# Performance work log

Hardware: AMD Instinct MI355X
Metric: run time of the kernel (lower is better)

The kernel has to match this reference:

```python
import jax, jax.numpy as jnp
import numpy as np

B, S, D_IN = 2, 2048, 2048
N_HEADS, N_KV, HEAD_DIM = 16, 4, 128
GROUP = N_HEADS // N_KV  # 4
SCALING = 256.0 ** -0.5  # query_pre_attn_scalar = 256
EPS = 1e-6


def rms_norm(x, scale):
    # RMSNorm over last dim (head_dim)
    var = jnp.mean(jnp.square(x), axis=-1, keepdims=True)
    return x * jax.lax.rsqrt(var + EPS) * scale


def apply_rope(x, cos, sin):
    # x: [b, h, s, d]; cos/sin: [s, d]
    d = x.shape[-1]
    x1, x2 = x[..., : d // 2], x[..., d // 2 :]
    rotated = jnp.concatenate([-x2, x1], axis=-1)
    return x * cos[None, None, :, :] + rotated * sin[None, None, :, :]


def setup_inputs() -> dict:
    key = jax.random.key(0)
    ks = jax.random.split(key, 6)
    x = jax.random.normal(ks[0], (B, S, D_IN), dtype=jnp.float32)
    Wq = jax.random.normal(ks[1], (D_IN, N_HEADS * HEAD_DIM), dtype=jnp.float32) * 0.02
    Wk = jax.random.normal(ks[2], (D_IN, N_KV * HEAD_DIM), dtype=jnp.float32) * 0.02
    Wv = jax.random.normal(ks[3], (D_IN, N_KV * HEAD_DIM), dtype=jnp.float32) * 0.02
    Wo = jax.random.normal(ks[4], (N_HEADS * HEAD_DIM, D_IN), dtype=jnp.float32) * 0.02
    q_scale = jnp.ones((HEAD_DIM,), dtype=jnp.float32)
    k_scale = jnp.ones((HEAD_DIM,), dtype=jnp.float32)
    # RoPE tables: angles repeated twice across head_dim
    inv_freq = 1.0 / (10000.0 ** (np.arange(0, HEAD_DIM, 2, dtype=np.float32) / HEAD_DIM))
    angles = np.arange(S, dtype=np.float32)[:, None] * inv_freq[None, :]  # [S, d/2]
    angles = np.concatenate([angles, angles], axis=-1)  # [S, d]
    cos = jnp.asarray(np.cos(angles), dtype=jnp.float32)
    sin = jnp.asarray(np.sin(angles), dtype=jnp.float32)
    # causal mask: True = masked (future positions)
    mask = jnp.triu(jnp.ones((S, S), dtype=bool), k=1)
    return {"x": x, "mask": mask, "cos": cos, "sin": sin,
            "Wq": Wq, "Wk": Wk, "Wv": Wv, "Wo": Wo,
            "q_scale": q_scale, "k_scale": k_scale}


def reference(x, mask, cos, sin, Wq, Wk, Wv, Wo, q_scale, k_scale):
    b, s, _ = x.shape
    q = (x @ Wq).reshape(b, s, N_HEADS, HEAD_DIM).transpose(0, 2, 1, 3)  # [b,h,s,d]
    k = (x @ Wk).reshape(b, s, N_KV, HEAD_DIM).transpose(0, 2, 1, 3)     # [b,g,s,d]
    v = (x @ Wv).reshape(b, s, N_KV, HEAD_DIM).transpose(0, 2, 1, 3)
    # qk-norm
    q = rms_norm(q, q_scale)
    k = rms_norm(k, k_scale)
    # RoPE
    q = apply_rope(q, cos, sin)
    k = apply_rope(k, cos, sin)
    # repeat KV across groups
    k = jnp.repeat(k, GROUP, axis=1)  # [b,h,s,d]
    v = jnp.repeat(v, GROUP, axis=1)
    q = q * SCALING
    scores = jnp.einsum('bhqd,bhkd->bhqk', q, k)
    scores = jnp.where(mask, -jnp.inf, scores)
    weights = jax.nn.softmax(scores, axis=-1)
    ctx = jnp.einsum('bhqk,bhkd->bhqd', weights, v)
    ctx = ctx.transpose(0, 2, 1, 3).reshape(b, s, N_HEADS * HEAD_DIM)
    return ctx @ Wo
```

## Files before the change

### kernel.cpp

```cpp
#include <hip/hip_runtime.h>
#include <hip/hip_bf16.h>


using u16 = unsigned short;
using u32 = unsigned int;

constexpr int Ss  = 2048;
constexpr int Hh  = 16;
constexpr int KVH = 4;

typedef __attribute__((ext_vector_type(8))) short bf16x8;
typedef __attribute__((ext_vector_type(4))) float f32x4;

__device__ inline float b2f(u16 v)  { return __uint_as_float(((u32)v) << 16); }
__device__ inline u16 f2bf(float x) {
  u32 u = __float_as_uint(x);
  return (u16)((u + 0x7fffu + ((u >> 16) & 1u)) >> 16);
}

typedef const __attribute__((address_space(1))) unsigned int gas_u32;
typedef __attribute__((address_space(3))) unsigned int las_u32;
__device__ inline void gl16(const void* g, void* l) {
  __builtin_amdgcn_global_load_lds((gas_u32*)g, (las_u32*)l, 16, 0, 0);
}

__global__ __launch_bounds__(256) void cvt_bf16(const float* __restrict__ in,
                                                u16* __restrict__ out, int n4) {
  int i = blockIdx.x * 256 + threadIdx.x;
  if (i < n4) {
    float4 f = reinterpret_cast<const float4*>(in)[i];
    ushort4 o;
    o.x = f2bf(f.x); o.y = f2bf(f.y); o.z = f2bf(f.z); o.w = f2bf(f.w);
    reinterpret_cast<ushort4*>(out)[i] = o;
  }
}

__global__ __launch_bounds__(256) void tcvt(const float* __restrict__ in,
                                            u16* __restrict__ out, int N, int K) {
  __shared__ u16 T[64][66];
  const int k0 = blockIdx.x * 64, n0 = blockIdx.y * 64;
  const int c = threadIdx.x & 63, rb = threadIdx.x >> 6;
#pragma unroll
  for (int p = 0; p < 16; p++) {
    int r = p * 4 + rb;
    T[c][r] = f2bf(in[(size_t)(k0 + r) * N + n0 + c]);
  }
  __syncthreads();
#pragma unroll
  for (int p = 0; p < 16; p++) {
    int nr = p * 4 + rb;
    out[(size_t)(n0 + nr) * K + k0 + c] = T[nr][c];
  }
}

__global__ __launch_bounds__(256) void vtrans(const u16* __restrict__ kv,
                                              u16* __restrict__ vT) {
  __shared__ u16 T[64][66];
  const int s0 = blockIdx.x * 64, d0 = blockIdx.y * 64, z = blockIdx.z;
  const int b = z >> 2, kvh = z & 3;
  const int c = threadIdx.x & 63, rb = threadIdx.x >> 6;
#pragma unroll
  for (int p = 0; p < 16; p++) {
    int r = p * 4 + rb;
    T[c][r] = kv[(size_t)(b * Ss + s0 + r) * 1024 + 512 + kvh * 128 + d0 + c];
  }
  __syncthreads();
#pragma unroll
  for (int p = 0; p < 16; p++) {
    int dr = p * 4 + rb;
    vT[((size_t)z * 128 + d0 + dr) * Ss + s0 + c] = T[dr][c];
  }
}

template <int OUT_F32>
__global__ __launch_bounds__(256) void gemm_bt(const u16* __restrict__ A,
                                               const u16* __restrict__ Bt,
                                               void* __restrict__ C,
                                               int N, int K) {
  __shared__ u16 As[128 * 64];
  __shared__ u16 Bs[128 * 64];
  const int t = threadIdx.x, w = t >> 6, lane = t & 63;
  const int lrow = lane & 15, quad = lane >> 4;
  const int wm = w & 1, wn = w >> 1;
  const int m0 = blockIdx.x * 128, n0 = blockIdx.y * 128;

  f32x4 acc[4][4];
#pragma unroll
  for (int i = 0; i < 4; i++)
#pragma unroll
    for (int j = 0; j < 4; j++) acc[i][j] = (f32x4)0.f;

  const int srow = t >> 3;
  const int scol = (t & 7) * 8;

  for (int k0 = 0; k0 < K; k0 += 64) {
#pragma unroll
    for (int c = 0; c < 4; c++) {
      gl16(A + (size_t)(m0 + c * 32 + srow) * K + k0 + scol,
           (char*)As + c * 4096 + t * 16);
      gl16(Bt + (size_t)(n0 + c * 32 + srow) * K + k0 + scol,
           (char*)Bs + c * 4096 + t * 16);
    }
    __syncthreads();
#pragma unroll
    for (int kc = 0; kc < 2; kc++) {
      bf16x8 af[4], bfr[4];
#pragma unroll
      for (int i = 0; i < 4; i++) {
        af[i] = *reinterpret_cast<const bf16x8*>(
            &As[(wm * 64 + i * 16 + lrow) * 64 + kc * 32 + quad * 8]);
        bfr[i] = *reinterpret_cast<const bf16x8*>(
            &Bs[(wn * 64 + i * 16 + lrow) * 64 + kc * 32 + quad * 8]);
      }
#pragma unroll
      for (int mi = 0; mi < 4; mi++)
#pragma unroll
        for (int ni = 0; ni < 4; ni++)
          acc[mi][ni] =
              __builtin_amdgcn_mfma_f32_16x16x32_bf16(af[mi], bfr[ni], acc[mi][ni], 0, 0, 0);
    }
    __syncthreads();
  }

#pragma unroll
  for (int mi = 0; mi < 4; mi++)
#pragma unroll
    for (int ni = 0; ni < 4; ni++)
#pragma unroll
      for (int r = 0; r < 4; r++) {
        int row = m0 + wm * 64 + mi * 16 + quad * 4 + r;
        int col = n0 + wn * 64 + ni * 16 + lrow;
        if (OUT_F32)
          reinterpret_cast<float*>(C)[(size_t)row * N + col] = acc[mi][ni][r];
        else
          reinterpret_cast<u16*>(C)[(size_t)row * N + col] = f2bf(acc[mi][ni][r]);
      }
}

__global__ __launch_bounds__(256) void rmsrope2(u16* __restrict__ qbuf,
                                                u16* __restrict__ kvb,
                                                const float* __restrict__ qsc,
                                                const float* __restrict__ ksc,
                                                const float* __restrict__ cosb,
                                                const float* __restrict__ sinb) {
  const int w = threadIdx.x >> 6, lane = threadIdx.x & 63;
  const int vi = blockIdx.x * 4 + w;
  const int tok = vi / 20, j = vi - tok * 20;
  const int s = tok & (Ss - 1);
  const bool isq = j < 16;
  u16* p = isq ? (qbuf + (size_t)tok * 2048 + j * 128)
               : (kvb + (size_t)tok * 1024 + (j - 16) * 128);
  const float* scale = isq ? qsc : ksc;
  const float mult = isq ? 0.0625f : 1.0f;
  float e0 = b2f(p[lane]), e1 = b2f(p[lane + 64]);
  float ss = e0 * e0 + e1 * e1;
#pragma unroll
  for (int off = 32; off > 0; off >>= 1) ss += __shfl_xor(ss, off);
  float rr = rsqrtf(ss * (1.0f / 128.0f) + 1e-6f);
  float x0 = e0 * rr * scale[lane];
  float x1 = e1 * rr * scale[lane + 64];
  float c0 = cosb[s * 128 + lane], c1 = cosb[s * 128 + 64 + lane];
  float sn0 = sinb[s * 128 + lane], sn1 = sinb[s * 128 + 64 + lane];
  p[lane]      = f2bf((x0 * c0 - x1 * sn0) * mult);
  p[lane + 64] = f2bf((x1 * c1 + x0 * sn1) * mult);
}

__global__ __launch_bounds__(256, 2) void attn_mfma(const u16* __restrict__ qb,
                                                    const u16* __restrict__ kv,
                                                    const u16* __restrict__ vT,
                                                    u16* __restrict__ ctx) {
  __shared__ u16 Ks[2][64 * 128];
  __shared__ u16 Vs[2][128 * 64];
  __shared__ u16 Ps[4][32 * 40];
  const int i = blockIdx.x;
  const int qt = (i < 256) ? (15 - (i >> 5)) : ((i - 256) >> 5);
  const int hb = i & 31;
  const int h = hb & 15, b = hb >> 4;
  const int t = threadIdx.x, w = t >> 6, lane = t & 63;
  const int lrow = lane & 15, quad = lane >> 4;
  const int kvh = h >> 2;
  const int qw = qt * 128 + w * 32;

  const u16* kbase = kv + (size_t)b * Ss * 1024 + kvh * 128;
  const u16* vbase = vT + (size_t)(b * KVH + kvh) * 128 * Ss;

  const int kr  = t >> 4;
  const int kco = ((t & 15) ^ (kr & 7)) * 8;
  const int vr  = t >> 3;
  const int vco = ((t & 7) ^ (vr & 7)) * 8;
  const int sw8 = (lrow & 7) << 3;

  bf16x8 qf[2][4];
#pragma unroll
  for (int g = 0; g < 2; g++)
#pragma unroll
    for (int c = 0; c < 4; c++)
      qf[g][c] = *reinterpret_cast<const bf16x8*>(
          qb + ((size_t)(b * Ss + qw + g * 16 + lrow) * Hh + h) * 128 + c * 32 + quad * 8);

  f32x4 o[2][8];
#pragma unroll
  for (int g = 0; g < 2; g++)
#pragma unroll
    for (int n = 0; n < 8; n++) o[g][n] = (f32x4)0.f;
  float mx[2] = {-1e30f, -1e30f}, ls[2] = {0.f, 0.f};

  const int ntile = 2 * qt + 2;

#pragma unroll
  for (int p = 0; p < 4; p++) {
    gl16(kbase + (size_t)(p * 16 + kr) * 1024 + kco,
         (char*)Ks[0] + (p * 256 + t) * 16);
    gl16(vbase + (size_t)(p * 32 + vr) * Ss + vco,
         (char*)Vs[0] + (p * 256 + t) * 16);
  }
  __syncthreads();

  int cur = 0;
  for (int kt = 0; kt < ntile; kt++) {
    const int kb0 = kt * 64;
    if (kt + 1 < ntile) {
      const int nb0 = kb0 + 64;
#pragma unroll
      for (int p = 0; p < 4; p++) {
        gl16(kbase + (size_t)(nb0 + p * 16 + kr) * 1024 + kco,
             (char*)Ks[cur ^ 1] + (p * 256 + t) * 16);
        gl16(vbase + (size_t)(p * 32 + vr) * Ss + nb0 + vco,
             (char*)Vs[cur ^ 1] + (p * 256 + t) * 16);
      }
    }

    if (kb0 <= qw + 31) {
      f32x4 st[2][4];
#pragma unroll
      for (int g = 0; g < 2; g++)
#pragma unroll
        for (int mt = 0; mt < 4; mt++) st[g][mt] = (f32x4)0.f;
#pragma unroll
      for (int c = 0; c < 4; c++) {
        bf16x8 kf[4];
#pragma unroll
        for (int mt = 0; mt < 4; mt++)
          kf[mt] = *reinterpret_cast<const bf16x8*>(
              &Ks[cur][(mt * 16 + lrow) * 128 + ((((c * 4 + quad) << 3)) ^ sw8)]);
        __builtin_amdgcn_s_setprio(1);
#pragma unroll
        for (int mt = 0; mt < 4; mt++)
#pragma unroll
          for (int g = 0; g < 2; g++)
            st[g][mt] =
                __builtin_amdgcn_mfma_f32_16x16x32_bf16(kf[mt], qf[g][c], st[g][mt], 0, 0, 0);
        __builtin_amdgcn_s_setprio(0);
      }
      if (kb0 + 63 > qw) {
#pragma unroll
        for (int g = 0; g < 2; g++) {
          int qg = qw + g * 16 + lrow;
#pragma unroll
          for (int mt = 0; mt < 4; mt++) {
            int kg = kb0 + mt * 16 + quad * 4;
#pragma unroll
            for (int r = 0; r < 4; r++)
              st[g][mt][r] = (kg + r > qg) ? -1e30f : st[g][mt][r];
          }
        }
      }
      float alpha[2];
#pragma unroll
      for (int g = 0; g < 2; g++) {
        f32x4 m4;
#pragma unroll
        for (int r = 0; r < 4; r++)
          m4[r] = fmaxf(fmaxf(st[g][0][r], st[g][1][r]), fmaxf(st[g][2][r], st[g][3][r]));
        float tm = fmaxf(fmaxf(m4[0], m4[1]), fmaxf(m4[2], m4[3]));
        tm = fmaxf(tm, __shfl_xor(tm, 16));
        tm = fmaxf(tm, __shfl_xor(tm, 32));
        float mn = fmaxf(mx[g], tm);
        alpha[g] = __expf(mx[g] - mn);
        mx[g] = mn;
        float tsum = 0.f;
#pragma unroll
        for (int mt = 0; mt < 4; mt++)
#pragma unroll
          for (int r = 0; r < 4; r++) {
            float pv = __expf(st[g][mt][r] - mn);
            st[g][mt][r] = pv;
            tsum += pv;
          }
        tsum += __shfl_xor(tsum, 16);
        tsum += __shfl_xor(tsum, 32);
        ls[g] = ls[g] * alpha[g] + tsum;
      }
#pragma unroll
      for (int g = 0; g < 2; g++)
#pragma unroll
        for (int n = 0; n < 8; n++) o[g][n] *= alpha[g];
#pragma unroll
      for (int c2 = 0; c2 < 2; c2++) {
#pragma unroll
        for (int g = 0; g < 2; g++)
#pragma unroll
          for (int mh = 0; mh < 2; mh++) {
            const f32x4 sv = st[g][c2 * 2 + mh];
            ushort4 pk;
            pk.x = f2bf(sv[0]); pk.y = f2bf(sv[1]);
            pk.z = f2bf(sv[2]); pk.w = f2bf(sv[3]);
            *reinterpret_cast<ushort4*>(
                &Ps[w][(g * 16 + lrow) * 40 + mh * 16 + quad * 4]) = pk;
          }
        bf16x8 pfr[2];
#pragma unroll
        for (int g = 0; g < 2; g++)
          pfr[g] = *reinterpret_cast<const bf16x8*>(
              &Ps[w][(g * 16 + lrow) * 40 + quad * 8]);
        __builtin_amdgcn_s_setprio(1);
#pragma unroll
        for (int n = 0; n < 8; n++) {
          bf16x8 vf = *reinterpret_cast<const bf16x8*>(
              &Vs[cur][(n * 16 + lrow) * 64 + ((((c2 * 4 + quad) << 3)) ^ sw8)]);
#pragma unroll
          for (int g = 0; g < 2; g++)
            o[g][n] = __builtin_amdgcn_mfma_f32_16x16x32_bf16(vf, pfr[g], o[g][n], 0, 0, 0);
        }
        __builtin_amdgcn_s_setprio(0);
      }
    }

    __syncthreads();
    cur ^= 1;
  }

#pragma unroll
  for (int g = 0; g < 2; g++) {
    float linv = 1.0f / ls[g];
    u16* obase = ctx + ((size_t)(b * Ss + qw + g * 16 + lrow) * Hh + h) * 128 + quad * 4;
#pragma unroll
    for (int n = 0; n < 8; n++) {
      ushort4 pk;
      pk.x = f2bf(o[g][n][0] * linv);
      pk.y = f2bf(o[g][n][1] * linv);
      pk.z = f2bf(o[g][n][2] * linv);
      pk.w = f2bf(o[g][n][3] * linv);
      *reinterpret_cast<ushort4*>(obase + n * 16) = pk;
    }
  }
}

extern "C" void kernel_launch(void* const* d_in, const int* in_sizes, int n_in,
                              void* d_out, int out_size, void* d_ws, size_t ws_size,
                              hipStream_t stream) {
  const float* x    = (const float*)d_in[0];
  const float* cosb = (const float*)d_in[2];
  const float* sinb = (const float*)d_in[3];
  const float* Wq   = (const float*)d_in[4];
  const float* Wk   = (const float*)d_in[5];
  const float* Wv   = (const float*)d_in[6];
  const float* Wo   = (const float*)d_in[7];
  const float* qsc  = (const float*)d_in[8];
  const float* ksc  = (const float*)d_in[9];

  const int M = 2 * Ss;
  u16* xb   = (u16*)d_ws;
  u16* ctxb = xb;
  u16* Wt   = xb + (size_t)8388608;
  u16* qbuf = Wt + (size_t)4194304;
  u16* kvb  = qbuf + (size_t)8388608;
  u16* vTb  = kvb + (size_t)4194304;

  cvt_bf16<<<8192, 256, 0, stream>>>(x, xb, 2097152);

  tcvt<<<dim3(32, 32), 256, 0, stream>>>(Wq, Wt, 2048, 2048);
  gemm_bt<0><<<dim3(32, 16), 256, 0, stream>>>(xb, Wt, qbuf, 2048, 2048);

  tcvt<<<dim3(32, 8), 256, 0, stream>>>(Wk, Wt, 512, 2048);
  tcvt<<<dim3(32, 8), 256, 0, stream>>>(Wv, Wt + (size_t)512 * 2048, 512, 2048);
  gemm_bt<0><<<dim3(32, 8), 256, 0, stream>>>(xb, Wt, kvb, 1024, 2048);

  rmsrope2<<<(M * 20) / 4, 256, 0, stream>>>(qbuf, kvb, qsc, ksc, cosb, sinb);

  vtrans<<<dim3(32, 2, 8), 256, 0, stream>>>(kvb, vTb);

  attn_mfma<<<dim3(512), 256, 0, stream>>>(qbuf, kvb, vTb, ctxb);

  tcvt<<<dim3(32, 32), 256, 0, stream>>>(Wo, Wt, 2048, 2048);
  gemm_bt<1><<<dim3(32, 16), 256, 0, stream>>>(ctxb, Wt, d_out, 2048, 2048);
}
```

Before: 388.0 us.

## Restructure attention into smaller blocks, lazy softmax rescale, packed bf16 conversion

Attention blocks shrink from 256 to 128 threads with 64-query tiles, and the grid doubles to 1024 blocks using a new causal load-balancing order. The K/V double buffer becomes a single-buffer load bracketed by two barriers. The online softmax now skips rescaling the output and row sum unless the running max grows by more than 8. Float-to-bf16 rounding uses the hardware packed conversion instruction. The aim is better occupancy, balance and fewer VALU ops, at the cost of exposed load latency from dropping the prefetch.

```diff
diff --git a/kernel.cpp b/kernel.cpp
--- a/kernel.cpp
+++ b/kernel.cpp
@@ -16,6 +16,11 @@
 __device__ inline u16 f2bf(float x) {
   u32 u = __float_as_uint(x);
   return (u16)((u + 0x7fffu + ((u >> 16) & 1u)) >> 16);
+}
+__device__ inline u32 cvtpk(float lo, float hi) {
+  u32 r;
+  asm("v_cvt_pk_bf16_f32 %0, %1, %2" : "=v"(r) : "v"(lo), "v"(hi));
+  return r;
 }
 
 typedef const __attribute__((address_space(1))) unsigned int gas_u32;
@@ -165,21 +170,21 @@
   p[lane + 64] = f2bf((x1 * c1 + x0 * sn1) * mult);
 }
 
-__global__ __launch_bounds__(256, 2) void attn_mfma(const u16* __restrict__ qb,
+__global__ __launch_bounds__(128, 2) void attn_mfma(const u16* __restrict__ qb,
                                                     const u16* __restrict__ kv,
                                                     const u16* __restrict__ vT,
                                                     u16* __restrict__ ctx) {
-  __shared__ u16 Ks[2][64 * 128];
-  __shared__ u16 Vs[2][128 * 64];
-  __shared__ u16 Ps[4][32 * 40];
+  __shared__ u16 Ks[64 * 128];
+  __shared__ u16 Vs[128 * 64];
+  __shared__ u16 Ps[2][32 * 40];
   const int i = blockIdx.x;
-  const int qt = (i < 256) ? (15 - (i >> 5)) : ((i - 256) >> 5);
-  const int hb = i & 31;
+  const int kq = i >> 8, jj = i & 255, x = jj >> 5, hb = jj & 31;
+  const int qtile = (kq == 0) ? 31 - x : (kq == 1) ? x : (kq == 2) ? 23 - x : 8 + x;
   const int h = hb & 15, b = hb >> 4;
   const int t = threadIdx.x, w = t >> 6, lane = t & 63;
   const int lrow = lane & 15, quad = lane >> 4;
   const int kvh = h >> 2;
-  const int qw = qt * 128 + w * 32;
+  const int qw = qtile * 64 + w * 32;
 
   const u16* kbase = kv + (size_t)b * Ss * 1024 + kvh * 128;
   const u16* vbase = vT + (size_t)(b * KVH + kvh) * 128 * Ss;
@@ -205,129 +210,120 @@
     for (int n = 0; n < 8; n++) o[g][n] = (f32x4)0.f;
   float mx[2] = {-1e30f, -1e30f}, ls[2] = {0.f, 0.f};
 
-  const int ntile = 2 * qt + 2;
-
-#pragma unroll
-  for (int p = 0; p < 4; p++) {
-    gl16(kbase + (size_t)(p * 16 + kr) * 1024 + kco,
-         (char*)Ks[0] + (p * 256 + t) * 16);
-    gl16(vbase + (size_t)(p * 32 + vr) * Ss + vco,
-         (char*)Vs[0] + (p * 256 + t) * 16);
-  }
-  __syncthreads();
-
-  int cur = 0;
+  const int ntile = qtile + 1;
   for (int kt = 0; kt < ntile; kt++) {
     const int kb0 = kt * 64;
-    if (kt + 1 < ntile) {
-      const int nb0 = kb0 + 64;
-#pragma unroll
-      for (int p = 0; p < 4; p++) {
-        gl16(kbase + (size_t)(nb0 + p * 16 + kr) * 1024 + kco,
-             (char*)Ks[cur ^ 1] + (p * 256 + t) * 16);
-        gl16(vbase + (size_t)(p * 32 + vr) * Ss + nb0 + vco,
-             (char*)Vs[cur ^ 1] + (p * 256 + t) * 16);
-      }
-    }
-
-    if (kb0 <= qw + 31) {
-      f32x4 st[2][4];
+    __syncthreads();
+#pragma unroll
+    for (int p8 = 0; p8 < 8; p8++) {
+      gl16(kbase + (size_t)(kb0 + p8 * 8 + kr) * 1024 + kco,
+           (char*)Ks + (p8 * 128 + t) * 16);
+      gl16(vbase + (size_t)(p8 * 16 + vr) * Ss + kb0 + vco,
+           (char*)Vs + (p8 * 128 + t) * 16);
+    }
+    __syncthreads();
+
+    f32x4 st[2][4];
+#pragma unroll
+    for (int g = 0; g < 2; g++)
+#pragma unroll
+      for (int mt = 0; mt < 4; mt++) st[g][mt] = (f32x4)0.f;
+#pragma unroll
+    for (int c = 0; c < 4; c++) {
+      bf16x8 kf[4];
+#pragma unroll
+      for (int mt = 0; mt < 4; mt++)
+        kf[mt] = *reinterpret_cast<const bf16x8*>(
+            &Ks[(mt * 16 + lrow) * 128 + ((((c * 4 + quad) << 3)) ^ sw8)]);
+      __builtin_amdgcn_s_setprio(1);
+#pragma unroll
+      for (int mt = 0; mt < 4; mt++)
+#pragma unroll
+        for (int g = 0; g < 2; g++)
+          st[g][mt] =
+              __builtin_amdgcn_mfma_f32_16x16x32_bf16(kf[mt], qf[g][c], st[g][mt], 0, 0, 0);
+      __builtin_amdgcn_s_setprio(0);
+    }
+    if (kb0 + 63 > qw) {
+#pragma unroll
+      for (int g = 0; g < 2; g++) {
+        int qg = qw + g * 16 + lrow;
+#pragma unroll
+        for (int mt = 0; mt < 4; mt++) {
+          int kg = kb0 + mt * 16 + quad * 4;
+#pragma unroll
+          for (int r = 0; r < 4; r++)
+            st[g][mt][r] = (kg + r > qg) ? -1e30f : st[g][mt][r];
+        }
+      }
+    }
+    float tmv[2];
+#pragma unroll
+    for (int g = 0; g < 2; g++) {
+      f32x4 m4;
+#pragma unroll
+      for (int r = 0; r < 4; r++)
+        m4[r] = fmaxf(fmaxf(st[g][0][r], st[g][1][r]), fmaxf(st[g][2][r], st[g][3][r]));
+      float tm = fmaxf(fmaxf(m4[0], m4[1]), fmaxf(m4[2], m4[3]));
+      tm = fmaxf(tm, __shfl_xor(tm, 16));
+      tm = fmaxf(tm, __shfl_xor(tm, 32));
+      tmv[g] = tm;
+    }
+    if (__any((tmv[0] > mx[0] + 8.0f) || (tmv[1] > mx[1] + 8.0f))) {
+#pragma unroll
+      for (int g = 0; g < 2; g++) {
+        float mn = fmaxf(mx[g], tmv[g]);
+        float a = __expf(mx[g] - mn);
+        mx[g] = mn;
+        ls[g] *= a;
+#pragma unroll
+        for (int n = 0; n < 8; n++) o[g][n] *= a;
+      }
+    }
+#pragma unroll
+    for (int g = 0; g < 2; g++) {
+      float tsum = 0.f;
+#pragma unroll
+      for (int mt = 0; mt < 4; mt++)
+#pragma unroll
+        for (int r = 0; r < 4; r++) {
+          float pv = __expf(st[g][mt][r] - mx[g]);
+          st[g][mt][r] = pv;
+          tsum += pv;
+        }
+      tsum += __shfl_xor(tsum, 16);
+      tsum += __shfl_xor(tsum, 32);
+      ls[g] += tsum;
+    }
+#pragma unroll
+    for (int c2 = 0; c2 < 2; c2++) {
 #pragma unroll
       for (int g = 0; g < 2; g++)
 #pragma unroll
-        for (int mt = 0; mt < 4; mt++) st[g][mt] = (f32x4)0.f;
-#pragma unroll
-      for (int c = 0; c < 4; c++) {
-        bf16x8 kf[4];
-#pragma unroll
-        for (int mt = 0; mt < 4; mt++)
-          kf[mt] = *reinterpret_cast<const bf16x8*>(
-              &Ks[cur][(mt * 16 + lrow) * 128 + ((((c * 4 + quad) << 3)) ^ sw8)]);
-        __builtin_amdgcn_s_setprio(1);
-#pragma unroll
-        for (int mt = 0; mt < 4; mt++)
-#pragma unroll
-          for (int g = 0; g < 2; g++)
-            st[g][mt] =
-                __builtin_amdgcn_mfma_f32_16x16x32_bf16(kf[mt], qf[g][c], st[g][mt], 0, 0, 0);
-        __builtin_amdgcn_s_setprio(0);
-      }
-      if (kb0 + 63 > qw) {
-#pragma unroll
-        for (int g = 0; g < 2; g++) {
-          int qg = qw + g * 16 + lrow;
-#pragma unroll
-          for (int mt = 0; mt < 4; mt++) {
-            int kg = kb0 + mt * 16 + quad * 4;
-#pragma unroll
-            for (int r = 0; r < 4; r++)
-              st[g][mt][r] = (kg + r > qg) ? -1e30f : st[g][mt][r];
-          }
+        for (int mh = 0; mh < 2; mh++) {
+          const f32x4 sv = st[g][c2 * 2 + mh];
+          uint2 pk;
+          pk.x = cvtpk(sv[0], sv[1]);
+          pk.y = cvtpk(sv[2], sv[3]);
+          *reinterpret_cast<uint2*>(
+              &Ps[w][(g * 16 + lrow) * 40 + mh * 16 + quad * 4]) = pk;
         }
-      }
-      float alpha[2];
-#pragma unroll
-      for (int g = 0; g < 2; g++) {
-        f32x4 m4;
-#pragma unroll
-        for (int r = 0; r < 4; r++)
-          m4[r] = fmaxf(fmaxf(st[g][0][r], st[g][1][r]), fmaxf(st[g][2][r], st[g][3][r]));
-        float tm = fmaxf(fmaxf(m4[0], m4[1]), fmaxf(m4[2], m4[3]));
-        tm = fmaxf(tm, __shfl_xor(tm, 16));
-        tm = fmaxf(tm, __shfl_xor(tm, 32));
-        float mn = fmaxf(mx[g], tm);
-        alpha[g] = __expf(mx[g] - mn);
-        mx[g] = mn;
-        float tsum = 0.f;
-#pragma unroll
-        for (int mt = 0; mt < 4; mt++)
-#pragma unroll
-          for (int r = 0; r < 4; r++) {
-            float pv = __expf(st[g][mt][r] - mn);
-            st[g][mt][r] = pv;
-            tsum += pv;
-          }
-        tsum += __shfl_xor(tsum, 16);
-        tsum += __shfl_xor(tsum, 32);
-        ls[g] = ls[g] * alpha[g] + tsum;
-      }
+      bf16x8 pfr[2];
 #pragma unroll
       for (int g = 0; g < 2; g++)
-#pragma unroll
-        for (int n = 0; n < 8; n++) o[g][n] *= alpha[g];
-#pragma unroll
-      for (int c2 = 0; c2 < 2; c2++) {
+        pfr[g] = *reinterpret_cast<const bf16x8*>(
+            &Ps[w][(g * 16 + lrow) * 40 + quad * 8]);
+      __builtin_amdgcn_s_setprio(1);
+#pragma unroll
+      for (int n = 0; n < 8; n++) {
+        bf16x8 vf = *reinterpret_cast<const bf16x8*>(
+            &Vs[(n * 16 + lrow) * 64 + ((((c2 * 4 + quad) << 3)) ^ sw8)]);
 #pragma unroll
         for (int g = 0; g < 2; g++)
-#pragma unroll
-          for (int mh = 0; mh < 2; mh++) {
-            const f32x4 sv = st[g][c2 * 2 + mh];
-            ushort4 pk;
-            pk.x = f2bf(sv[0]); pk.y = f2bf(sv[1]);
-            pk.z = f2bf(sv[2]); pk.w = f2bf(sv[3]);
-            *reinterpret_cast<ushort4*>(
-                &Ps[w][(g * 16 + lrow) * 40 + mh * 16 + quad * 4]) = pk;
-          }
-        bf16x8 pfr[2];
-#pragma unroll
-        for (int g = 0; g < 2; g++)
-          pfr[g] = *reinterpret_cast<const bf16x8*>(
-              &Ps[w][(g * 16 + lrow) * 40 + quad * 8]);
-        __builtin_amdgcn_s_setprio(1);
-#pragma unroll
-        for (int n = 0; n < 8; n++) {
-          bf16x8 vf = *reinterpret_cast<const bf16x8*>(
-              &Vs[cur][(n * 16 + lrow) * 64 + ((((c2 * 4 + quad) << 3)) ^ sw8)]);
-#pragma unroll
-          for (int g = 0; g < 2; g++)
-            o[g][n] = __builtin_amdgcn_mfma_f32_16x16x32_bf16(vf, pfr[g], o[g][n], 0, 0, 0);
-        }
-        __builtin_amdgcn_s_setprio(0);
-      }
-    }
-
-    __syncthreads();
-    cur ^= 1;
+          o[g][n] = __builtin_amdgcn_mfma_f32_16x16x32_bf16(vf, pfr[g], o[g][n], 0, 0, 0);
+      }
+      __builtin_amdgcn_s_setprio(0);
+    }
   }
 
 #pragma unroll
@@ -336,12 +332,10 @@
     u16* obase = ctx + ((size_t)(b * Ss + qw + g * 16 + lrow) * Hh + h) * 128 + quad * 4;
 #pragma unroll
     for (int n = 0; n < 8; n++) {
-      ushort4 pk;
-      pk.x = f2bf(o[g][n][0] * linv);
-      pk.y = f2bf(o[g][n][1] * linv);
-      pk.z = f2bf(o[g][n][2] * linv);
-      pk.w = f2bf(o[g][n][3] * linv);
-      *reinterpret_cast<ushort4*>(obase + n * 16) = pk;
+      uint2 pk;
+      pk.x = cvtpk(o[g][n][0] * linv, o[g][n][1] * linv);
+      pk.y = cvtpk(o[g][n][2] * linv, o[g][n][3] * linv);
+      *reinterpret_cast<uint2*>(obase + n * 16) = pk;
     }
   }
 }
@@ -380,7 +374,7 @@
 
   vtrans<<<dim3(32, 2, 8), 256, 0, stream>>>(kvb, vTb);
 
-  attn_mfma<<<dim3(512), 256, 0, stream>>>(qbuf, kvb, vTb, ctxb);
+  attn_mfma<<<dim3(1024), 128, 0, stream>>>(qbuf, kvb, vTb, ctxb);
 
   tcvt<<<dim3(32, 32), 256, 0, stream>>>(Wo, Wt, 2048, 2048);
   gemm_bt<1><<<dim3(32, 16), 256, 0, stream>>>(ctxb, Wt, d_out, 2048, 2048);
```

Measured after the change: 382.3 us. About the same (-1.5%).
